# Optimization experiments

Hardware: AMD Instinct MI355X
Metric: run time of the kernel (lower is better)

## Reference

```python
import jax, jax.numpy as jnp
import numpy as np

B, NQ, NK, D = 64, 1024, 1024, 128
MASK_VALUE = -1e6


def setup_inputs() -> dict:
    key = jax.random.key(0)
    kq, kk, kv, kl = jax.random.split(key, 4)
    queries = jax.random.normal(kq, (B, NQ, D), dtype=jnp.float32)
    keys = jax.random.normal(kk, (B, NK, D), dtype=jnp.float32)
    values = jax.random.normal(kv, (B, NK, D), dtype=jnp.float32)
    valid_lens = jax.random.randint(kl, (B,), 1, NK + 1, dtype=jnp.int32)
    return {"queries": queries, "keys": keys, "values": values, "valid_lens": valid_lens}


def reference(queries, keys, values, valid_lens):
    d = queries.shape[-1]
    # scores: [B, Nq, Nk]
    scores = jnp.einsum("bqd,bkd->bqk", queries, keys) / jnp.sqrt(jnp.float32(d))
    # valid_lens [B] -> mask over last (key) axis, same for every query row
    key_pos = jnp.arange(scores.shape[-1])  # [Nk]
    mask = key_pos[None, None, :] < valid_lens[:, None, None]  # [B,1,Nk] broadcast
    scores = jnp.where(mask, scores, jnp.float32(MASK_VALUE))
    attn = jax.nn.softmax(scores, axis=-1)
    # dropout p=0.0 (eval): identity
    return jnp.einsum("bqk,bkd->bqd", attn, values)
```

## Files before the change

kernel.cpp:

```cpp
#include <hip/hip_runtime.h>

typedef __bf16 bf16x8 __attribute__((ext_vector_type(8)));
typedef __bf16 bf16x2 __attribute__((ext_vector_type(2)));
typedef float f32x4 __attribute__((ext_vector_type(4)));
typedef float f32x16 __attribute__((ext_vector_type(16)));
typedef int i32x4 __attribute__((ext_vector_type(4)));

namespace {
constexpr int kNQ = 1024;
constexpr int kNK = 1024;
constexpr int kD = 128;
constexpr int kBK = 32;
constexpr int kTileElems = 4096;
constexpr float kScaleLog2e = 0.12751742f;
}

__device__ __forceinline__ int packbf(float a, float b) {
    bf16x2 t; t[0] = (__bf16)a; t[1] = (__bf16)b;
    return __builtin_bit_cast(int, t);
}

__device__ __forceinline__ void async16(const __bf16* g, const __bf16* l) {
    __builtin_amdgcn_global_load_lds(
        (const __attribute__((address_space(1))) void*)g,
        (__attribute__((address_space(3))) void*)l, 16, 0, 0);
}

__global__ void repack(const float* __restrict__ K, const float* __restrict__ V,
                       const int* __restrict__ VL,
                       __bf16* __restrict__ Kimg, __bf16* __restrict__ Vimg,
                       int* __restrict__ perm) {
    const int blk = blockIdx.x;

    if (blk == 64 * 32) {
        const int t = threadIdx.x;
        if (t < 64) {
            const int v = VL[t];
            int rank = 0;
            for (int j = 0; j < 64; ++j) {
                const int vj = VL[j];
                rank += (vj > v) || (vj == v && j < t);
            }
            perm[rank] = t;
        }
        return;
    }

    const int b = blk >> 5, t = blk & 31;
    if (t * kBK >= VL[b]) return;
    const int tid = threadIdx.x;
    __shared__ float vbuf[32 * 132];

    const size_t tileofs = (size_t)(b * 32 + t) * kTileElems;

    #pragma unroll
    for (int it = 0; it < 2; ++it) {
        const int chunk = tid + it * 256;
        const int k = chunk >> 4;
        const int p = chunk & 15;
        const int c = p ^ (k & 15);
        const float* src = K + (((size_t)b * kNK + t * kBK + k) * kD + c * 8);
        const f32x4 x0 = *(const f32x4*)src;
        const f32x4 x1 = *(const f32x4*)(src + 4);
        bf16x8 h;
        #pragma unroll
        for (int j = 0; j < 4; ++j) { h[j] = (__bf16)x0[j]; h[4 + j] = (__bf16)x1[j]; }
        *(bf16x8*)(Kimg + tileofs + chunk * 8) = h;
    }

    {
        const int r = tid >> 3, col0 = (tid & 7) * 16;
        const float* src = V + (((size_t)b * kNK + t * kBK + r) * kD + col0);
        #pragma unroll
        for (int j = 0; j < 4; ++j) {
            const f32x4 x = *(const f32x4*)(src + j * 4);
            *(f32x4*)&vbuf[r * 132 + col0 + j * 4] = x;
        }
    }
    __syncthreads();
    #pragma unroll
    for (int it = 0; it < 2; ++it) {
        const int chunk = tid + it * 256;
        const int d = chunk >> 2;
        const int p = chunk & 3;
        const int q = p ^ ((d >> 1) & 3);
        bf16x8 h;
        #pragma unroll
        for (int j = 0; j < 8; ++j) h[j] = (__bf16)vbuf[(q * 8 + j) * 132 + d];
        *(bf16x8*)(Vimg + tileofs + chunk * 8) = h;
    }
}

__global__ __launch_bounds__(256, 2)
void fa_fwd(const float* __restrict__ Q, const int* __restrict__ VL,
            const int* __restrict__ perm, const __bf16* __restrict__ Kimg,
            const __bf16* __restrict__ Vimg, float* __restrict__ O)
{
    __shared__ __align__(16) __bf16 kls[4][kTileElems];
    __shared__ __align__(16) __bf16 vls[4][kTileElems];

    const int tid  = threadIdx.x;
    const int wave = tid >> 6;
    const int lane = tid & 63;
    const int key  = lane & 31;
    const int hi   = lane >> 5;

    const int i = blockIdx.x;
    const int j = i & 255;
    const int rank = (i >> 8) ? (511 - j) : j;

    const int b  = perm[rank >> 3];
    const int q0 = (rank & 7) * 128 + wave * 32;

    const int valid  = VL[b];
    const int ntiles = (valid + kBK - 1) / kBK;
    const size_t bT  = (size_t)b * 32;

    auto stage = [&](int slot, int t) {
        const __bf16* kg = Kimg + (bT + t) * kTileElems;
        const __bf16* vg = Vimg + (bT + t) * kTileElems;
        #pragma unroll
        for (int ii = 0; ii < 2; ++ii) {
            const int seg = wave * 1024 + ii * 512;
            async16(kg + seg + lane * 8, &kls[slot][seg]);
            async16(vg + seg + lane * 8, &vls[slot][seg]);
        }
    };

    stage(0, 0);
    if (ntiles > 1) stage(1, 1);

    bf16x8 qf[8];
    {
        const float* qp = Q + ((size_t)b * kNQ + q0 + key) * kD + hi * 8;
        #pragma unroll
        for (int s = 0; s < 8; ++s) {
            const f32x4 x0 = *(const f32x4*)(qp + s * 16);
            const f32x4 x1 = *(const f32x4*)(qp + s * 16 + 4);
            #pragma unroll
            for (int jj = 0; jj < 4; ++jj) {
                qf[s][jj]     = (__bf16)x0[jj];
                qf[s][4 + jj] = (__bf16)x1[jj];
            }
        }
    }

    f32x16 acc0, acc1, acc2, acc3;
    #pragma unroll
    for (int r = 0; r < 16; ++r) { acc0[r]=0.f; acc1[r]=0.f; acc2[r]=0.f; acc3[r]=0.f; }
    float lsum = 0.f;

    const int kterm = key & 15;
    const int vterm = (key >> 1) & 3;
    const int xaddr = (lane ^ 32) << 2;
    const int hi4   = hi << 2;

    for (int t = 0; t < ntiles; ++t) {
        if (t + 2 < ntiles) {
            stage((t + 2) & 3, t + 2);
            asm volatile("s_waitcnt vmcnt(8)" ::: "memory");
        } else if (t + 1 < ntiles) {
            asm volatile("s_waitcnt vmcnt(4)" ::: "memory");
        } else {
            asm volatile("s_waitcnt vmcnt(0)" ::: "memory");
        }
        __builtin_amdgcn_s_barrier();
        __builtin_amdgcn_sched_barrier(0);

        const __bf16* kbuf = kls[t & 3];
        const __bf16* vbuf = vls[t & 3];

        f32x16 sa, sb;
        #pragma unroll
        for (int r = 0; r < 16; ++r) { sa[r] = 0.f; sb[r] = 0.f; }
        __builtin_amdgcn_s_setprio(1);
        #pragma unroll
        for (int s = 0; s < 4; ++s) {
            const bf16x8 kf = *(const bf16x8*)&kbuf[key * 128 + (((s * 2 + hi) ^ kterm) << 3)];
            sa = __builtin_amdgcn_mfma_f32_32x32x16_bf16(kf, qf[s], sa, 0, 0, 0);
        }
        #pragma unroll
        for (int s = 4; s < 8; ++s) {
            const bf16x8 kf = *(const bf16x8*)&kbuf[key * 128 + (((s * 2 + hi) ^ kterm) << 3)];
            sb = __builtin_amdgcn_mfma_f32_32x32x16_bf16(kf, qf[s], sb, 0, 0, 0);
        }
        __builtin_amdgcn_s_setprio(0);
        f32x16 sv = sa + sb;

        const int kb = t * kBK;
        if (kb + kBK > valid) {
            #pragma unroll
            for (int r = 0; r < 16; ++r) {
                const int cr = (r & 3) + 8 * (r >> 2);
                if (kb + cr + hi4 >= valid) sv[r] = -1e30f;
            }
        }

        #pragma unroll
        for (int r = 0; r < 16; ++r) sv[r] = __builtin_amdgcn_exp2f(sv[r] * kScaleLog2e);

        {
            float a0 = sv[0]+sv[1], a1 = sv[2]+sv[3], a2 = sv[4]+sv[5], a3 = sv[6]+sv[7];
            float a4 = sv[8]+sv[9], a5 = sv[10]+sv[11], a6 = sv[12]+sv[13], a7 = sv[14]+sv[15];
            lsum += ((a0+a1)+(a2+a3)) + ((a4+a5)+(a6+a7));
        }

        int w[8], pw[8];
        #pragma unroll
        for (int jp = 0; jp < 8; ++jp) w[jp] = packbf(sv[2*jp], sv[2*jp+1]);
        #pragma unroll
        for (int jp = 0; jp < 8; ++jp) pw[jp] = __builtin_amdgcn_ds_bpermute(xaddr, w[jp]);

        i32x4 f0, f1;
        f0[0] = hi ? pw[2] : w[0];
        f0[1] = hi ? pw[3] : w[1];
        f0[2] = hi ? w[2]  : pw[0];
        f0[3] = hi ? w[3]  : pw[1];
        f1[0] = hi ? pw[6] : w[4];
        f1[1] = hi ? pw[7] : w[5];
        f1[2] = hi ? w[6]  : pw[4];
        f1[3] = hi ? w[7]  : pw[5];
        const bf16x8 pfs0 = __builtin_bit_cast(bf16x8, f0);
        const bf16x8 pfs1 = __builtin_bit_cast(bf16x8, f1);

        __builtin_amdgcn_s_setprio(1);
        {
            const int vb0 = key * 32 + (((0 + hi) ^ vterm) << 3);
            const int vb1 = key * 32 + (((2 + hi) ^ vterm) << 3);
            const bf16x8 v00 = *(const bf16x8*)&vbuf[0 * 1024 + vb0];
            const bf16x8 v10 = *(const bf16x8*)&vbuf[1 * 1024 + vb0];
            const bf16x8 v20 = *(const bf16x8*)&vbuf[2 * 1024 + vb0];
            const bf16x8 v30 = *(const bf16x8*)&vbuf[3 * 1024 + vb0];
            acc0 = __builtin_amdgcn_mfma_f32_32x32x16_bf16(pfs0, v00, acc0, 0, 0, 0);
            acc1 = __builtin_amdgcn_mfma_f32_32x32x16_bf16(pfs0, v10, acc1, 0, 0, 0);
            acc2 = __builtin_amdgcn_mfma_f32_32x32x16_bf16(pfs0, v20, acc2, 0, 0, 0);
            acc3 = __builtin_amdgcn_mfma_f32_32x32x16_bf16(pfs0, v30, acc3, 0, 0, 0);
            const bf16x8 v01 = *(const bf16x8*)&vbuf[0 * 1024 + vb1];
            const bf16x8 v11 = *(const bf16x8*)&vbuf[1 * 1024 + vb1];
            const bf16x8 v21 = *(const bf16x8*)&vbuf[2 * 1024 + vb1];
            const bf16x8 v31 = *(const bf16x8*)&vbuf[3 * 1024 + vb1];
            acc0 = __builtin_amdgcn_mfma_f32_32x32x16_bf16(pfs1, v01, acc0, 0, 0, 0);
            acc1 = __builtin_amdgcn_mfma_f32_32x32x16_bf16(pfs1, v11, acc1, 0, 0, 0);
            acc2 = __builtin_amdgcn_mfma_f32_32x32x16_bf16(pfs1, v21, acc2, 0, 0, 0);
            acc3 = __builtin_amdgcn_mfma_f32_32x32x16_bf16(pfs1, v31, acc3, 0, 0, 0);
        }
        __builtin_amdgcn_s_setprio(0);
    }

    const int plb = __builtin_amdgcn_ds_bpermute(xaddr, __builtin_bit_cast(int, lsum));
    const float linv = 1.0f / (lsum + __builtin_bit_cast(float, plb));
    float* ob = O + ((size_t)b * kNQ + q0) * kD;
    const int hib = hi << 4;
    #pragma unroll
    for (int r = 0; r < 16; ++r) {
        const int cr = (r & 3) + 8 * (r >> 2);
        const int iv = __builtin_amdgcn_ds_bpermute((cr << 2) + hib,
                                                    __builtin_bit_cast(int, linv));
        const float inv = __builtin_bit_cast(float, iv);
        const int q = cr + hi4;
        ob[q * kD +   0 + key] = acc0[r] * inv;
        ob[q * kD +  32 + key] = acc1[r] * inv;
        ob[q * kD +  64 + key] = acc2[r] * inv;
        ob[q * kD +  96 + key] = acc3[r] * inv;
    }
}

extern "C" void kernel_launch(void* const* d_in, const int* in_sizes, int n_in,
                              void* d_out, int out_size, void* d_ws, size_t ws_size,
                              hipStream_t stream) {
    const float* Q = (const float*)d_in[0];
    const float* K = (const float*)d_in[1];
    const float* V = (const float*)d_in[2];
    const int*  VL = (const int*)d_in[3];
    float* O = (float*)d_out;

    int* perm = (int*)d_ws;
    __bf16* Kimg = (__bf16*)((char*)d_ws + 4096);
    __bf16* Vimg = (__bf16*)((char*)d_ws + 4096 + (size_t)16 * 1024 * 1024);

    repack<<<dim3(64 * 32 + 1), 256, 0, stream>>>(K, V, VL, Kimg, Vimg, perm);
    fa_fwd<<<dim3(512), 256, 0, stream>>>(Q, VL, perm, Kimg, Vimg, O);
}
```

Baseline: 169.2 us.

## Load K/V fragments directly from global into registers, dropping LDS staging

The repack kernel now writes K and V tiles in MFMA-fragment order, so each lane reads its bf16x8 operand contiguously. The attention kernel stops staging tiles through shared memory with async global-to-LDS copies and barriers. Each wave instead loads the next tile's K and V fragments straight into registers, one tile ahead. This removes LDS traffic and block barriers, but every wave now reads K/V from global or cache separately, with only a one-tile prefetch distance and higher register pressure.

```diff
diff --git a/kernel.cpp b/kernel.cpp
--- a/kernel.cpp
+++ b/kernel.cpp
@@ -18,12 +18,6 @@
 __device__ __forceinline__ int packbf(float a, float b) {
     bf16x2 t; t[0] = (__bf16)a; t[1] = (__bf16)b;
     return __builtin_bit_cast(int, t);
-}
-
-__device__ __forceinline__ void async16(const __bf16* g, const __bf16* l) {
-    __builtin_amdgcn_global_load_lds(
-        (const __attribute__((address_space(1))) void*)g,
-        (__attribute__((address_space(3))) void*)l, 16, 0, 0);
 }
 
 __global__ void repack(const float* __restrict__ K, const float* __restrict__ V,
@@ -53,19 +47,21 @@
 
     const size_t tileofs = (size_t)(b * 32 + t) * kTileElems;
 
-    #pragma unroll
-    for (int it = 0; it < 2; ++it) {
-        const int chunk = tid + it * 256;
-        const int k = chunk >> 4;
-        const int p = chunk & 15;
-        const int c = p ^ (k & 15);
-        const float* src = K + (((size_t)b * kNK + t * kBK + k) * kD + c * 8);
-        const f32x4 x0 = *(const f32x4*)src;
+    {
+        const int key = tid >> 3, s = tid & 7;
+        const float* src = K + (((size_t)b * kNK + t * kBK + key) * kD + s * 16);
+        const f32x4 x0 = *(const f32x4*)(src + 0);
         const f32x4 x1 = *(const f32x4*)(src + 4);
-        bf16x8 h;
-        #pragma unroll
-        for (int j = 0; j < 4; ++j) { h[j] = (__bf16)x0[j]; h[4 + j] = (__bf16)x1[j]; }
-        *(bf16x8*)(Kimg + tileofs + chunk * 8) = h;
+        const f32x4 x2 = *(const f32x4*)(src + 8);
+        const f32x4 x3 = *(const f32x4*)(src + 12);
+        bf16x8 h0, h1;
+        #pragma unroll
+        for (int j = 0; j < 4; ++j) {
+            h0[j] = (__bf16)x0[j]; h0[4 + j] = (__bf16)x1[j];
+            h1[j] = (__bf16)x2[j]; h1[4 + j] = (__bf16)x3[j];
+        }
+        *(bf16x8*)(Kimg + tileofs + (s * 64 + key) * 8)      = h0;
+        *(bf16x8*)(Kimg + tileofs + (s * 64 + 32 + key) * 8) = h1;
     }
 
     {
@@ -80,14 +76,17 @@
     __syncthreads();
     #pragma unroll
     for (int it = 0; it < 2; ++it) {
-        const int chunk = tid + it * 256;
-        const int d = chunk >> 2;
-        const int p = chunk & 3;
-        const int q = p ^ ((d >> 1) & 3);
+        const int ch  = tid + it * 256;
+        const int db  = ch >> 7;
+        const int s   = (ch >> 6) & 1;
+        const int hi  = (ch >> 5) & 1;
+        const int key = ch & 31;
+        const int d   = db * 32 + key;
+        const int k8  = s * 16 + hi * 8;
         bf16x8 h;
         #pragma unroll
-        for (int j = 0; j < 8; ++j) h[j] = (__bf16)vbuf[(q * 8 + j) * 132 + d];
-        *(bf16x8*)(Vimg + tileofs + chunk * 8) = h;
+        for (int j = 0; j < 8; ++j) h[j] = (__bf16)vbuf[(k8 + j) * 132 + d];
+        *(bf16x8*)(Vimg + tileofs + ch * 8) = h;
     }
 }
 
@@ -96,9 +95,6 @@
             const int* __restrict__ perm, const __bf16* __restrict__ Kimg,
             const __bf16* __restrict__ Vimg, float* __restrict__ O)
 {
-    __shared__ __align__(16) __bf16 kls[4][kTileElems];
-    __shared__ __align__(16) __bf16 vls[4][kTileElems];
-
     const int tid  = threadIdx.x;
     const int wave = tid >> 6;
     const int lane = tid & 63;
@@ -114,21 +110,9 @@
 
     const int valid  = VL[b];
     const int ntiles = (valid + kBK - 1) / kBK;
-    const size_t bT  = (size_t)b * 32;
-
-    auto stage = [&](int slot, int t) {
-        const __bf16* kg = Kimg + (bT + t) * kTileElems;
-        const __bf16* vg = Vimg + (bT + t) * kTileElems;
-        #pragma unroll
-        for (int ii = 0; ii < 2; ++ii) {
-            const int seg = wave * 1024 + ii * 512;
-            async16(kg + seg + lane * 8, &kls[slot][seg]);
-            async16(vg + seg + lane * 8, &vls[slot][seg]);
-        }
-    };
-
-    stage(0, 0);
-    if (ntiles > 1) stage(1, 1);
+    const __bf16* kbase = Kimg + (size_t)b * 32 * kTileElems;
+    const __bf16* vbase = Vimg + (size_t)b * 32 * kTileElems;
+    const int fofs = lane * 8;
 
     bf16x8 qf[8];
     {
@@ -145,46 +129,42 @@
         }
     }
 
+    bf16x8 kr[8], vr[8];
+    #pragma unroll
+    for (int s = 0; s < 8; ++s)
+        kr[s] = *(const bf16x8*)(kbase + s * 512 + fofs);
+    #pragma unroll
+    for (int f = 0; f < 8; ++f)
+        vr[f] = *(const bf16x8*)(vbase + f * 512 + fofs);
+
     f32x16 acc0, acc1, acc2, acc3;
     #pragma unroll
     for (int r = 0; r < 16; ++r) { acc0[r]=0.f; acc1[r]=0.f; acc2[r]=0.f; acc3[r]=0.f; }
     float lsum = 0.f;
 
-    const int kterm = key & 15;
-    const int vterm = (key >> 1) & 3;
     const int xaddr = (lane ^ 32) << 2;
     const int hi4   = hi << 2;
 
     for (int t = 0; t < ntiles; ++t) {
-        if (t + 2 < ntiles) {
-            stage((t + 2) & 3, t + 2);
-            asm volatile("s_waitcnt vmcnt(8)" ::: "memory");
-        } else if (t + 1 < ntiles) {
-            asm volatile("s_waitcnt vmcnt(4)" ::: "memory");
-        } else {
-            asm volatile("s_waitcnt vmcnt(0)" ::: "memory");
-        }
-        __builtin_amdgcn_s_barrier();
-        __builtin_amdgcn_sched_barrier(0);
-
-        const __bf16* kbuf = kls[t & 3];
-        const __bf16* vbuf = vls[t & 3];
-
         f32x16 sa, sb;
         #pragma unroll
         for (int r = 0; r < 16; ++r) { sa[r] = 0.f; sb[r] = 0.f; }
         __builtin_amdgcn_s_setprio(1);
         #pragma unroll
-        for (int s = 0; s < 4; ++s) {
-            const bf16x8 kf = *(const bf16x8*)&kbuf[key * 128 + (((s * 2 + hi) ^ kterm) << 3)];
-            sa = __builtin_amdgcn_mfma_f32_32x32x16_bf16(kf, qf[s], sa, 0, 0, 0);
-        }
-        #pragma unroll
-        for (int s = 4; s < 8; ++s) {
-            const bf16x8 kf = *(const bf16x8*)&kbuf[key * 128 + (((s * 2 + hi) ^ kterm) << 3)];
-            sb = __builtin_amdgcn_mfma_f32_32x32x16_bf16(kf, qf[s], sb, 0, 0, 0);
-        }
+        for (int s = 0; s < 4; ++s)
+            sa = __builtin_amdgcn_mfma_f32_32x32x16_bf16(kr[s], qf[s], sa, 0, 0, 0);
+        #pragma unroll
+        for (int s = 4; s < 8; ++s)
+            sb = __builtin_amdgcn_mfma_f32_32x32x16_bf16(kr[s], qf[s], sb, 0, 0, 0);
         __builtin_amdgcn_s_setprio(0);
+
+        if (t + 1 < ntiles) {
+            const __bf16* kt = kbase + (size_t)(t + 1) * kTileElems;
+            #pragma unroll
+            for (int s = 0; s < 8; ++s)
+                kr[s] = *(const bf16x8*)(kt + s * 512 + fofs);
+        }
+
         f32x16 sv = sa + sb;
 
         const int kb = t * kBK;
@@ -224,27 +204,22 @@
         const bf16x8 pfs1 = __builtin_bit_cast(bf16x8, f1);
 
         __builtin_amdgcn_s_setprio(1);
-        {
-            const int vb0 = key * 32 + (((0 + hi) ^ vterm) << 3);
-            const int vb1 = key * 32 + (((2 + hi) ^ vterm) << 3);
-            const bf16x8 v00 = *(const bf16x8*)&vbuf[0 * 1024 + vb0];
-            const bf16x8 v10 = *(const bf16x8*)&vbuf[1 * 1024 + vb0];
-            const bf16x8 v20 = *(const bf16x8*)&vbuf[2 * 1024 + vb0];
-            const bf16x8 v30 = *(const bf16x8*)&vbuf[3 * 1024 + vb0];
-            acc0 = __builtin_amdgcn_mfma_f32_32x32x16_bf16(pfs0, v00, acc0, 0, 0, 0);
-            acc1 = __builtin_amdgcn_mfma_f32_32x32x16_bf16(pfs0, v10, acc1, 0, 0, 0);
-            acc2 = __builtin_amdgcn_mfma_f32_32x32x16_bf16(pfs0, v20, acc2, 0, 0, 0);
-            acc3 = __builtin_amdgcn_mfma_f32_32x32x16_bf16(pfs0, v30, acc3, 0, 0, 0);
-            const bf16x8 v01 = *(const bf16x8*)&vbuf[0 * 1024 + vb1];
-            const bf16x8 v11 = *(const bf16x8*)&vbuf[1 * 1024 + vb1];
-            const bf16x8 v21 = *(const bf16x8*)&vbuf[2 * 1024 + vb1];
-            const bf16x8 v31 = *(const bf16x8*)&vbuf[3 * 1024 + vb1];
-            acc0 = __builtin_amdgcn_mfma_f32_32x32x16_bf16(pfs1, v01, acc0, 0, 0, 0);
-            acc1 = __builtin_amdgcn_mfma_f32_32x32x16_bf16(pfs1, v11, acc1, 0, 0, 0);
-            acc2 = __builtin_amdgcn_mfma_f32_32x32x16_bf16(pfs1, v21, acc2, 0, 0, 0);
-            acc3 = __builtin_amdgcn_mfma_f32_32x32x16_bf16(pfs1, v31, acc3, 0, 0, 0);
-        }
+        acc0 = __builtin_amdgcn_mfma_f32_32x32x16_bf16(pfs0, vr[0], acc0, 0, 0, 0);
+        acc1 = __builtin_amdgcn_mfma_f32_32x32x16_bf16(pfs0, vr[2], acc1, 0, 0, 0);
+        acc2 = __builtin_amdgcn_mfma_f32_32x32x16_bf16(pfs0, vr[4], acc2, 0, 0, 0);
+        acc3 = __builtin_amdgcn_mfma_f32_32x32x16_bf16(pfs0, vr[6], acc3, 0, 0, 0);
+        acc0 = __builtin_amdgcn_mfma_f32_32x32x16_bf16(pfs1, vr[1], acc0, 0, 0, 0);
+        acc1 = __builtin_amdgcn_mfma_f32_32x32x16_bf16(pfs1, vr[3], acc1, 0, 0, 0);
+        acc2 = __builtin_amdgcn_mfma_f32_32x32x16_bf16(pfs1, vr[5], acc2, 0, 0, 0);
+        acc3 = __builtin_amdgcn_mfma_f32_32x32x16_bf16(pfs1, vr[7], acc3, 0, 0, 0);
         __builtin_amdgcn_s_setprio(0);
+
+        if (t + 1 < ntiles) {
+            const __bf16* vt = vbase + (size_t)(t + 1) * kTileElems;
+            #pragma unroll
+            for (int f = 0; f < 8; ++f)
+                vr[f] = *(const bf16x8*)(vt + f * 512 + fofs);
+        }
     }
 
     const int plb = __builtin_amdgcn_ds_bpermute(xaddr, __builtin_bit_cast(int, lsum));
```

Result: faster. 163.5 us (-3.4%).
